# Performance work log

Hardware: AMD Instinct MI355X
Metric: run time of the kernel (lower is better)

Reference implementation:

```python
import jax, jax.numpy as jnp
import numpy as np

CONTEXT_SIZE = 256  # hardcoded in source; scale = context_size**-0.5, not head_size
EMBED_DIM = 384
HEAD_SIZE = 64
BATCH = 512
SEQ = 256


def setup_inputs() -> dict:
    key = jax.random.key(0)
    ks = jax.random.split(key, 7)
    s = 1.0 / np.sqrt(EMBED_DIM)
    return {
        "x": jax.random.normal(ks[0], (BATCH, SEQ, EMBED_DIM), jnp.float32),
        "Wq": jax.random.uniform(ks[1], (EMBED_DIM, HEAD_SIZE), jnp.float32, -s, s),
        "bq": jax.random.uniform(ks[2], (HEAD_SIZE,), jnp.float32, -s, s),
        "Wk": jax.random.uniform(ks[3], (EMBED_DIM, HEAD_SIZE), jnp.float32, -s, s),
        "bk": jax.random.uniform(ks[4], (HEAD_SIZE,), jnp.float32, -s, s),
        "Wv": jax.random.uniform(ks[5], (EMBED_DIM, HEAD_SIZE), jnp.float32, -s, s),
        "bv": jax.random.uniform(ks[6], (HEAD_SIZE,), jnp.float32, -s, s),
    }


def reference(x, Wq, bq, Wk, bk, Wv, bv):
    # x: [B, T, D]
    T = x.shape[1]
    q = x @ Wq + bq          # [B, T, H]
    k = x @ Wk + bk          # [B, T, H]
    v = x @ Wv + bv          # [B, T, H]
    scale = CONTEXT_SIZE ** (-0.5)  # faithful: source scales by context_size, not head_size
    scores = jnp.einsum("bth,bsh->bts", q, k) * scale  # [B, T, T]
    causal = jnp.tril(jnp.ones((T, T), dtype=bool))
    scores = jnp.where(causal, scores, -jnp.inf)
    attn = jax.nn.softmax(scores, axis=-1)
    # dropout omitted (eval mode / deterministic reference)
    return jnp.einsum("bts,bsh->bth", attn, v)  # [B, T, H]
```

## Files before the change

kernel.cpp:

```cpp
#include <hip/hip_runtime.h>
#include <hip/hip_bf16.h>
#include <stdint.h>

#define B_ 512
#define T_ 256
#define D_ 384
#define H_ 64

typedef __attribute__((ext_vector_type(8))) short bf16x8;
typedef __attribute__((ext_vector_type(4))) float f32x4;
typedef __attribute__((ext_vector_type(16))) float f32x16;

__device__ __forceinline__ unsigned short f2bf(float f) {
  union { float f; unsigned int u; } a; a.f = f;
  unsigned int r = (a.u + 0x7FFFu + ((a.u >> 16) & 1u)) >> 16;
  return (unsigned short)r;
}

__device__ __forceinline__ unsigned int pkbf(float lo, float hi) {
  unsigned int r;
  asm("v_cvt_pk_bf16_f32 %0, %1, %2" : "=v"(r) : "v"(lo), "v"(hi));
  return r;
}

__global__ void prep_wt(const float* __restrict__ Wq, const float* __restrict__ Wk,
                        const float* __restrict__ Wv, unsigned short* __restrict__ wt) {
  int idx = blockIdx.x * 256 + threadIdx.x;
  if (idx >= 192 * 384) return;
  int n = idx / 384, k = idx - n * 384;
  int sel = n >> 6, c = n & 63;
  const float* W = (sel == 0) ? Wq : ((sel == 1) ? Wk : Wv);
  wt[idx] = f2bf(W[k * 64 + c]);
}

__global__ __launch_bounds__(1024) void attn_fused(
    const float* __restrict__ x, const float* __restrict__ bq,
    const float* __restrict__ bk, const float* __restrict__ bv,
    const unsigned short* __restrict__ wt, float* __restrict__ out) {
  extern __shared__ char smem[];
  const int tid = threadIdx.x;
  const int b = blockIdx.x;
  const int wv = tid >> 6, lane = tid & 63;
  const int lo4 = lane & 15, hi4 = lane >> 4;
  const int lo5 = lane & 31, hi5 = lane >> 5;

  const float* xb = x + (size_t)b * T_ * D_;
  const int row0 = 16 * wv + lo4;

  f32x4 acc[12];
#pragma unroll
  for (int ct = 0; ct < 12; ++ct) acc[ct] = (f32x4)0.0f;

  for (int half = 0; half < 2; ++half) {
#pragma unroll
    for (int i = 0; i < 5; ++i) {
      int u = tid + 1024 * i;
      if (u < 4608) {
        int n = u / 24;
        int mp = u - n * 24;
        int m = mp ^ (n & 7);
        const uint4* src = reinterpret_cast<const uint4*>(wt + n * 384 + half * 192 + 8 * m);
        *reinterpret_cast<uint4*>(smem + 16 * u) = *src;
      }
    }
    __syncthreads();
#pragma unroll
    for (int ks6 = 0; ks6 < 6; ++ks6) {
      int ks = half * 6 + ks6;
      const float* p = xb + row0 * D_ + 32 * ks + 8 * hi4;
      float4 f0 = *reinterpret_cast<const float4*>(p);
      float4 f1 = *reinterpret_cast<const float4*>(p + 4);
      union { bf16x8 v; unsigned int w[4]; } A;
      A.w[0] = pkbf(f0.x, f0.y); A.w[1] = pkbf(f0.z, f0.w);
      A.w[2] = pkbf(f1.x, f1.y); A.w[3] = pkbf(f1.z, f1.w);
      bf16x8 afr = A.v;
#pragma unroll
      for (int ct = 0; ct < 12; ++ct) {
        int n = 16 * ct + lo4;
        int kbyte = (64 * ks6 + 16 * hi4) ^ ((n & 7) << 4);
        bf16x8 bw = *reinterpret_cast<const bf16x8*>(smem + n * 384 + kbyte);
        acc[ct] = __builtin_amdgcn_mfma_f32_16x16x32_bf16(afr, bw, acc[ct], 0, 0, 0);
      }
    }
    __syncthreads();
  }

#pragma unroll
  for (int ct = 0; ct < 12; ++ct) {
    int n = 16 * ct + lo4;
    float bias = (ct < 4) ? bq[n] : ((ct < 8) ? bk[n - 64] : bv[n - 128]);
    int rowb = 16 * wv + 4 * hi4;
#pragma unroll
    for (int r = 0; r < 4; ++r) {
      int row = rowb + r;
      unsigned short v = f2bf(acc[ct][r] + bias);
      if (ct < 4) {
        int h = n;
        *reinterpret_cast<unsigned short*>(smem + row * 128 + ((2 * h) ^ ((row & 7) << 4))) = v;
      } else if (ct < 8) {
        int h = n - 64;
        *reinterpret_cast<unsigned short*>(smem + 32768 + row * 128 + ((2 * h) ^ ((row & 7) << 4))) = v;
      } else {
        int h = n - 128;
        *reinterpret_cast<unsigned short*>(smem + 65536 + h * 512 + ((2 * row) ^ ((h & 7) << 4))) = v;
      }
    }
  }
  __syncthreads();

  if (wv < 8) {
    const float cexp = 0.09016844005555897f;

    bf16x8 qf[4];
    {
      int row = 32 * wv + lo5;
#pragma unroll
      for (int s = 0; s < 4; ++s)
        qf[s] = *reinterpret_cast<const bf16x8*>(
            smem + row * 128 + (((32 * s + 16 * hi5)) ^ ((row & 7) << 4)));
    }

    f32x16 o0 = (f32x16)0.0f, o1 = (f32x16)0.0f;
    float lsum = 0.0f;

    for (int kb = 0; kb <= wv; ++kb) {
      f32x16 st = (f32x16)0.0f;
      {
        int row = 32 * kb + lo5;
#pragma unroll
        for (int s = 0; s < 4; ++s) {
          bf16x8 kf = *reinterpret_cast<const bf16x8*>(
              smem + 32768 + row * 128 + (((32 * s + 16 * hi5)) ^ ((row & 7) << 4)));
          st = __builtin_amdgcn_mfma_f32_32x32x16_bf16(kf, qf[s], st, 0, 0, 0);
        }
      }
      float p[16];
#pragma unroll
      for (int r = 0; r < 16; ++r) {
        float e = exp2f(cexp * st[r]);
        if (kb == wv) {
          int keyl = (r & 3) + 8 * (r >> 2) + 4 * hi5;
          if (keyl > lo5) e = 0.0f;
        }
        p[r] = e;
        lsum += e;
      }

      union { bf16x8 v; unsigned int w[4]; } A0, A1;
      {
        unsigned int X0 = pkbf(p[0], p[1]),  X1 = pkbf(p[2], p[3]);
        unsigned int Y0 = pkbf(p[4], p[5]),  Y1 = pkbf(p[6], p[7]);
        unsigned int X0p = (unsigned int)__shfl_xor((int)X0, 32);
        unsigned int X1p = (unsigned int)__shfl_xor((int)X1, 32);
        unsigned int Y0p = (unsigned int)__shfl_xor((int)Y0, 32);
        unsigned int Y1p = (unsigned int)__shfl_xor((int)Y1, 32);
        A0.w[0] = hi5 ? Y0p : X0;
        A0.w[1] = hi5 ? Y1p : X1;
        A0.w[2] = hi5 ? Y0  : X0p;
        A0.w[3] = hi5 ? Y1  : X1p;
        unsigned int Z0 = pkbf(p[8], p[9]),   Z1 = pkbf(p[10], p[11]);
        unsigned int W0 = pkbf(p[12], p[13]), W1 = pkbf(p[14], p[15]);
        unsigned int Z0p = (unsigned int)__shfl_xor((int)Z0, 32);
        unsigned int Z1p = (unsigned int)__shfl_xor((int)Z1, 32);
        unsigned int W0p = (unsigned int)__shfl_xor((int)W0, 32);
        unsigned int W1p = (unsigned int)__shfl_xor((int)W1, 32);
        A1.w[0] = hi5 ? W0p : Z0;
        A1.w[1] = hi5 ? W1p : Z1;
        A1.w[2] = hi5 ? W0  : Z0p;
        A1.w[3] = hi5 ? W1  : Z1p;
      }
#pragma unroll
      for (int s2 = 0; s2 < 2; ++s2) {
        bf16x8 pa = s2 ? A1.v : A0.v;
        int kk = 32 * kb + 16 * s2 + 8 * hi5;
#pragma unroll
        for (int ht = 0; ht < 2; ++ht) {
          int h = 32 * ht + lo5;
          bf16x8 vf = *reinterpret_cast<const bf16x8*>(
              smem + 65536 + h * 512 + (((2 * kk)) ^ ((h & 7) << 4)));
          if (ht == 0) o0 = __builtin_amdgcn_mfma_f32_32x32x16_bf16(pa, vf, o0, 0, 0, 0);
          else         o1 = __builtin_amdgcn_mfma_f32_32x32x16_bf16(pa, vf, o1, 0, 0, 0);
        }
      }
    }

    lsum += __shfl_xor(lsum, 32);
    float inv = 1.0f / lsum;
    float* ob = out + (size_t)b * T_ * H_;
#pragma unroll
    for (int r = 0; r < 16; ++r) {
      int ridx = (r & 3) + 8 * (r >> 2) + 4 * hi5;
      float invr = __shfl(inv, ridx);
      int row = 32 * wv + ridx;
      ob[row * H_ + lo5]      = o0[r] * invr;
      ob[row * H_ + 32 + lo5] = o1[r] * invr;
    }
  }
}

extern "C" void kernel_launch(void* const* d_in, const int* in_sizes, int n_in,
                              void* d_out, int out_size, void* d_ws, size_t ws_size,
                              hipStream_t stream) {
  const float* x  = (const float*)d_in[0];
  const float* Wq = (const float*)d_in[1];
  const float* bq = (const float*)d_in[2];
  const float* Wk = (const float*)d_in[3];
  const float* bk = (const float*)d_in[4];
  const float* Wv = (const float*)d_in[5];
  const float* bv = (const float*)d_in[6];
  unsigned short* wt = (unsigned short*)d_ws;
  float* out = (float*)d_out;

  prep_wt<<<288, 256, 0, stream>>>(Wq, Wk, Wv, wt);
  attn_fused<<<B_, 1024, 98304, stream>>>(x, bq, bk, bv, wt, out);
}
```

Measured before the change: 63.66 us.

## Restructure QKV projection to stage x tiles in LDS with 2D warp tiling

Result: slower. 101.0 us (+58.7%).

```diff
diff --git a/kernel.cpp b/kernel.cpp
--- a/kernel.cpp
+++ b/kernel.cpp
@@ -6,6 +6,11 @@
 #define T_ 256
 #define D_ 384
 #define H_ 64
+
+#define XT_ 0
+#define WT_ 49152
+#define KK_ 89088
+#define VT_ 121856
 
 typedef __attribute__((ext_vector_type(8))) short bf16x8;
 typedef __attribute__((ext_vector_type(4))) float f32x4;
@@ -43,84 +48,104 @@
   const int wv = tid >> 6, lane = tid & 63;
   const int lo4 = lane & 15, hi4 = lane >> 4;
   const int lo5 = lane & 31, hi5 = lane >> 5;
-
-  const float* xb = x + (size_t)b * T_ * D_;
-  const int row0 = 16 * wv + lo4;
-
-  f32x4 acc[12];
-#pragma unroll
-  for (int ct = 0; ct < 12; ++ct) acc[ct] = (f32x4)0.0f;
-
-  for (int half = 0; half < 2; ++half) {
-#pragma unroll
-    for (int i = 0; i < 5; ++i) {
-      int u = tid + 1024 * i;
-      if (u < 4608) {
-        int n = u / 24;
-        int mp = u - n * 24;
-        int m = mp ^ (n & 7);
-        const uint4* src = reinterpret_cast<const uint4*>(wt + n * 384 + half * 192 + 8 * m);
-        *reinterpret_cast<uint4*>(smem + 16 * u) = *src;
+  const int rf = wv >> 2, cg = wv & 3;
+
+  const char* xb = (const char*)x + (size_t)b * T_ * D_ * 4;
+
+  bf16x8 qf[4];
+  f32x16 o0 = (f32x16)0.0f, o1 = (f32x16)0.0f;
+
+  for (int rt = 0; rt < 4; ++rt) {
+    f32x4 acc[3];
+#pragma unroll
+    for (int ci = 0; ci < 3; ++ci) acc[ci] = (f32x4)0.0f;
+
+    {
+      const char* base = xb + (size_t)rt * 64 * 1536;
+#pragma unroll
+      for (int i = 0; i < 3; ++i) {
+        int p = tid + 1024 * i;
+        float4 f0 = *reinterpret_cast<const float4*>(base + 32 * p);
+        float4 f1 = *reinterpret_cast<const float4*>(base + 32 * p + 16);
+        int row = p / 48;
+        int j = p - 48 * row;
+        union { uint4 v; unsigned int w[4]; } U;
+        U.w[0] = pkbf(f0.x, f0.y); U.w[1] = pkbf(f0.z, f0.w);
+        U.w[2] = pkbf(f1.x, f1.y); U.w[3] = pkbf(f1.z, f1.w);
+        *reinterpret_cast<uint4*>(smem + XT_ + row * 768 + ((16 * j) ^ ((row & 7) << 4))) = U.v;
       }
     }
     __syncthreads();
-#pragma unroll
-    for (int ks6 = 0; ks6 < 6; ++ks6) {
-      int ks = half * 6 + ks6;
-      const float* p = xb + row0 * D_ + 32 * ks + 8 * hi4;
-      float4 f0 = *reinterpret_cast<const float4*>(p);
-      float4 f1 = *reinterpret_cast<const float4*>(p + 4);
-      union { bf16x8 v; unsigned int w[4]; } A;
-      A.w[0] = pkbf(f0.x, f0.y); A.w[1] = pkbf(f0.z, f0.w);
-      A.w[2] = pkbf(f1.x, f1.y); A.w[3] = pkbf(f1.z, f1.w);
-      bf16x8 afr = A.v;
-#pragma unroll
-      for (int ct = 0; ct < 12; ++ct) {
-        int n = 16 * ct + lo4;
-        int kbyte = (64 * ks6 + 16 * hi4) ^ ((n & 7) << 4);
-        bf16x8 bw = *reinterpret_cast<const bf16x8*>(smem + n * 384 + kbyte);
-        acc[ct] = __builtin_amdgcn_mfma_f32_16x16x32_bf16(afr, bw, acc[ct], 0, 0, 0);
-      }
+
+    for (int qtr = 0; qtr < 4; ++qtr) {
+#pragma unroll
+      for (int i = 0; i < 3; ++i) {
+        int u = tid + 1024 * i;
+        if (u < 2496) {
+          int n = u / 13;
+          int c = u - 13 * n;
+          if (c < 12) {
+            uint4 v = *reinterpret_cast<const uint4*>(wt + n * 384 + 96 * qtr + 8 * c);
+            *reinterpret_cast<uint4*>(smem + WT_ + n * 208 + 16 * c) = v;
+          }
+        }
+      }
+      __syncthreads();
+#pragma unroll
+      for (int ks = 0; ks < 3; ++ks) {
+        int rowl = 16 * rf + lo4;
+        bf16x8 afr = *reinterpret_cast<const bf16x8*>(
+            smem + XT_ + rowl * 768 + (((192 * qtr + 64 * ks + 16 * hi4)) ^ ((rowl & 7) << 4)));
+#pragma unroll
+        for (int ci = 0; ci < 3; ++ci) {
+          int n = 16 * (3 * cg + ci) + lo4;
+          bf16x8 bw = *reinterpret_cast<const bf16x8*>(
+              smem + WT_ + n * 208 + 64 * ks + 16 * hi4);
+          acc[ci] = __builtin_amdgcn_mfma_f32_16x16x32_bf16(afr, bw, acc[ci], 0, 0, 0);
+        }
+      }
+      __syncthreads();
+    }
+
+#pragma unroll
+    for (int ci = 0; ci < 3; ++ci) {
+      int ct = 3 * cg + ci;
+      int n = 16 * ct + lo4;
+      float bias = (ct < 4) ? bq[n] : ((ct < 8) ? bk[n - 64] : bv[n - 128]);
+#pragma unroll
+      for (int r = 0; r < 4; ++r) {
+        int rowl = 16 * rf + 4 * hi4 + r;
+        int row = 64 * rt + rowl;
+        unsigned short v = f2bf(acc[ci][r] + bias);
+        if (ct < 4) {
+          int h = n;
+          *reinterpret_cast<unsigned short*>(
+              smem + XT_ + rowl * 128 + ((2 * h) ^ ((rowl & 7) << 4))) = v;
+        } else if (ct < 8) {
+          int h = n - 64;
+          *reinterpret_cast<unsigned short*>(
+              smem + KK_ + row * 128 + ((2 * h) ^ ((row & 7) << 4))) = v;
+        } else {
+          int h = n - 128;
+          *reinterpret_cast<unsigned short*>(
+              smem + VT_ + h * 512 + ((2 * row) ^ ((h & 7) << 4))) = v;
+        }
+      }
+    }
+    __syncthreads();
+
+    if ((wv >> 1) == rt) {
+      int rowl = 32 * (wv & 1) + lo5;
+#pragma unroll
+      for (int s = 0; s < 4; ++s)
+        qf[s] = *reinterpret_cast<const bf16x8*>(
+            smem + XT_ + rowl * 128 + (((32 * s + 16 * hi5)) ^ ((rowl & 7) << 4)));
     }
     __syncthreads();
   }
 
-#pragma unroll
-  for (int ct = 0; ct < 12; ++ct) {
-    int n = 16 * ct + lo4;
-    float bias = (ct < 4) ? bq[n] : ((ct < 8) ? bk[n - 64] : bv[n - 128]);
-    int rowb = 16 * wv + 4 * hi4;
-#pragma unroll
-    for (int r = 0; r < 4; ++r) {
-      int row = rowb + r;
-      unsigned short v = f2bf(acc[ct][r] + bias);
-      if (ct < 4) {
-        int h = n;
-        *reinterpret_cast<unsigned short*>(smem + row * 128 + ((2 * h) ^ ((row & 7) << 4))) = v;
-      } else if (ct < 8) {
-        int h = n - 64;
-        *reinterpret_cast<unsigned short*>(smem + 32768 + row * 128 + ((2 * h) ^ ((row & 7) << 4))) = v;
-      } else {
-        int h = n - 128;
-        *reinterpret_cast<unsigned short*>(smem + 65536 + h * 512 + ((2 * row) ^ ((h & 7) << 4))) = v;
-      }
-    }
-  }
-  __syncthreads();
-
   if (wv < 8) {
     const float cexp = 0.09016844005555897f;
-
-    bf16x8 qf[4];
-    {
-      int row = 32 * wv + lo5;
-#pragma unroll
-      for (int s = 0; s < 4; ++s)
-        qf[s] = *reinterpret_cast<const bf16x8*>(
-            smem + row * 128 + (((32 * s + 16 * hi5)) ^ ((row & 7) << 4)));
-    }
-
-    f32x16 o0 = (f32x16)0.0f, o1 = (f32x16)0.0f;
     float lsum = 0.0f;
 
     for (int kb = 0; kb <= wv; ++kb) {
@@ -130,7 +155,7 @@
 #pragma unroll
         for (int s = 0; s < 4; ++s) {
           bf16x8 kf = *reinterpret_cast<const bf16x8*>(
-              smem + 32768 + row * 128 + (((32 * s + 16 * hi5)) ^ ((row & 7) << 4)));
+              smem + KK_ + row * 128 + (((32 * s + 16 * hi5)) ^ ((row & 7) << 4)));
           st = __builtin_amdgcn_mfma_f32_32x32x16_bf16(kf, qf[s], st, 0, 0, 0);
         }
       }
@@ -177,7 +202,7 @@
         for (int ht = 0; ht < 2; ++ht) {
           int h = 32 * ht + lo5;
           bf16x8 vf = *reinterpret_cast<const bf16x8*>(
-              smem + 65536 + h * 512 + (((2 * kk)) ^ ((h & 7) << 4)));
+              smem + VT_ + h * 512 + (((2 * kk)) ^ ((h & 7) << 4)));
           if (ht == 0) o0 = __builtin_amdgcn_mfma_f32_32x32x16_bf16(pa, vf, o0, 0, 0, 0);
           else         o1 = __builtin_amdgcn_mfma_f32_32x32x16_bf16(pa, vf, o1, 0, 0, 0);
         }
@@ -212,5 +237,5 @@
   float* out = (float*)d_out;
 
   prep_wt<<<288, 256, 0, stream>>>(Wq, Wk, Wv, wt);
-  attn_fused<<<B_, 1024, 98304, stream>>>(x, bq, bk, bv, wt, out);
-}
+  attn_fused<<<B_, 1024, 154624, stream>>>(x, bq, bk, bv, wt, out);
+}
```

## Stream pre-tiled bf16 weights from global into 32x32 MFMA projection, dropping LDS staging

Applied to the files above, without the earlier changes.

Result: slower. 96.53 us (+51.6%).

```diff
diff --git a/kernel.cpp b/kernel.cpp
--- a/kernel.cpp
+++ b/kernel.cpp
@@ -8,7 +8,6 @@
 #define H_ 64
 
 typedef __attribute__((ext_vector_type(8))) short bf16x8;
-typedef __attribute__((ext_vector_type(4))) float f32x4;
 typedef __attribute__((ext_vector_type(16))) float f32x16;
 
 __device__ __forceinline__ unsigned short f2bf(float f) {
@@ -26,8 +25,12 @@
 __global__ void prep_wt(const float* __restrict__ Wq, const float* __restrict__ Wk,
                         const float* __restrict__ Wv, unsigned short* __restrict__ wt) {
   int idx = blockIdx.x * 256 + threadIdx.x;
-  if (idx >= 192 * 384) return;
-  int n = idx / 384, k = idx - n * 384;
+  if (idx >= 24 * 192 * 16) return;
+  int k16 = idx / 3072;
+  int rem = idx - k16 * 3072;
+  int n = rem >> 4;
+  int j = rem & 15;
+  int k = 16 * k16 + j;
   int sel = n >> 6, c = n & 63;
   const float* W = (sel == 0) ? Wq : ((sel == 1) ? Wk : Wv);
   wt[idx] = f2bf(W[k * 64 + c]);
@@ -41,68 +44,56 @@
   const int tid = threadIdx.x;
   const int b = blockIdx.x;
   const int wv = tid >> 6, lane = tid & 63;
-  const int lo4 = lane & 15, hi4 = lane >> 4;
   const int lo5 = lane & 31, hi5 = lane >> 5;
-
-  const float* xb = x + (size_t)b * T_ * D_;
-  const int row0 = 16 * wv + lo4;
-
-  f32x4 acc[12];
-#pragma unroll
-  for (int ct = 0; ct < 12; ++ct) acc[ct] = (f32x4)0.0f;
-
-  for (int half = 0; half < 2; ++half) {
-#pragma unroll
-    for (int i = 0; i < 5; ++i) {
-      int u = tid + 1024 * i;
-      if (u < 4608) {
-        int n = u / 24;
-        int mp = u - n * 24;
-        int m = mp ^ (n & 7);
-        const uint4* src = reinterpret_cast<const uint4*>(wt + n * 384 + half * 192 + 8 * m);
-        *reinterpret_cast<uint4*>(smem + 16 * u) = *src;
-      }
-    }
-    __syncthreads();
-#pragma unroll
-    for (int ks6 = 0; ks6 < 6; ++ks6) {
-      int ks = half * 6 + ks6;
-      const float* p = xb + row0 * D_ + 32 * ks + 8 * hi4;
-      float4 f0 = *reinterpret_cast<const float4*>(p);
-      float4 f1 = *reinterpret_cast<const float4*>(p + 4);
-      union { bf16x8 v; unsigned int w[4]; } A;
-      A.w[0] = pkbf(f0.x, f0.y); A.w[1] = pkbf(f0.z, f0.w);
-      A.w[2] = pkbf(f1.x, f1.y); A.w[3] = pkbf(f1.z, f1.w);
-      bf16x8 afr = A.v;
-#pragma unroll
-      for (int ct = 0; ct < 12; ++ct) {
-        int n = 16 * ct + lo4;
-        int kbyte = (64 * ks6 + 16 * hi4) ^ ((n & 7) << 4);
-        bf16x8 bw = *reinterpret_cast<const bf16x8*>(smem + n * 384 + kbyte);
-        acc[ct] = __builtin_amdgcn_mfma_f32_16x16x32_bf16(afr, bw, acc[ct], 0, 0, 0);
-      }
-    }
-    __syncthreads();
+  const int rg = wv >> 1, cg = wv & 1;
+
+  const char* xb = (const char*)x + (size_t)b * T_ * D_ * 4;
+  const int rowg = 32 * rg + lo5;
+  const char* xrow = xb + (size_t)rowg * 1536 + 32 * hi5;
+  const char* wbase = (const char*)wt + 3072 * cg + 32 * lo5 + 16 * hi5;
+
+  f32x16 acc[3];
+#pragma unroll
+  for (int ci = 0; ci < 3; ++ci) acc[ci] = (f32x16)0.0f;
+
+#pragma unroll 4
+  for (int w = 0; w < 24; ++w) {
+    float4 f0 = *reinterpret_cast<const float4*>(xrow + 64 * w);
+    float4 f1 = *reinterpret_cast<const float4*>(xrow + 64 * w + 16);
+    union { bf16x8 v; unsigned int u[4]; } A;
+    A.u[0] = pkbf(f0.x, f0.y); A.u[1] = pkbf(f0.z, f0.w);
+    A.u[2] = pkbf(f1.x, f1.y); A.u[3] = pkbf(f1.z, f1.w);
+    bf16x8 afr = A.v;
+#pragma unroll
+    for (int ci = 0; ci < 3; ++ci) {
+      bf16x8 bw = *reinterpret_cast<const bf16x8*>(wbase + 6144 * w + 1024 * ci);
+      acc[ci] = __builtin_amdgcn_mfma_f32_32x32x16_bf16(bw, afr, acc[ci], 0, 0, 0);
+    }
   }
 
 #pragma unroll
-  for (int ct = 0; ct < 12; ++ct) {
-    int n = 16 * ct + lo4;
-    float bias = (ct < 4) ? bq[n] : ((ct < 8) ? bk[n - 64] : bv[n - 128]);
-    int rowb = 16 * wv + 4 * hi4;
-#pragma unroll
-    for (int r = 0; r < 4; ++r) {
-      int row = rowb + r;
-      unsigned short v = f2bf(acc[ct][r] + bias);
-      if (ct < 4) {
-        int h = n;
-        *reinterpret_cast<unsigned short*>(smem + row * 128 + ((2 * h) ^ ((row & 7) << 4))) = v;
-      } else if (ct < 8) {
-        int h = n - 64;
-        *reinterpret_cast<unsigned short*>(smem + 32768 + row * 128 + ((2 * h) ^ ((row & 7) << 4))) = v;
-      } else {
-        int h = n - 128;
-        *reinterpret_cast<unsigned short*>(smem + 65536 + h * 512 + ((2 * row) ^ ((h & 7) << 4))) = v;
+  for (int ci = 0; ci < 3; ++ci) {
+    int nbase = 96 * cg + 32 * ci;
+    if (nbase < 128) {
+      const float* barr = (nbase < 64) ? bq : bk;
+      int cb = (nbase < 64) ? nbase : (nbase - 64);
+      char* basep = smem + ((nbase < 64) ? 0 : 32768);
+#pragma unroll
+      for (int rb = 0; rb < 4; ++rb) {
+        int c4 = cb + 8 * rb + 4 * hi5;
+        float4 b4 = *reinterpret_cast<const float4*>(barr + c4);
+        uint2 pv;
+        pv.x = pkbf(acc[ci][4 * rb + 0] + b4.x, acc[ci][4 * rb + 1] + b4.y);
+        pv.y = pkbf(acc[ci][4 * rb + 2] + b4.z, acc[ci][4 * rb + 3] + b4.w);
+        *reinterpret_cast<uint2*>(basep + rowg * 128 + ((2 * c4) ^ ((rowg & 7) << 4))) = pv;
+      }
+    } else {
+#pragma unroll
+      for (int r = 0; r < 16; ++r) {
+        int hh = nbase - 128 + (r & 3) + 8 * (r >> 2) + 4 * hi5;
+        unsigned short v = f2bf(acc[ci][r] + bv[hh]);
+        *reinterpret_cast<unsigned short*>(
+            smem + 65536 + hh * 512 + ((2 * rowg) ^ ((hh & 7) << 4))) = v;
       }
     }
   }
```
